# Optimization experiments

Measured on AMD Instinct MI355X. Metric: run time of the kernel, lower is better.

Reference implementation:

```python
import jax, jax.numpy as jnp
import numpy as np

B, T, D = 16, 4096, 768          # batch, tokens, hidden
N_BOX = 1024                      # total boxes across batch
MAX_BBOX = 128                    # cfg.MODEL.MAX_BBOX_NUM
DIM_DETR = 256                    # DETR feature dim (features[:,1:])


def _lin(k, din, dout):
    kw, kb = jax.random.split(k)
    s = 1.0 / np.sqrt(din)
    W = jax.random.uniform(kw, (dout, din), minval=-s, maxval=s, dtype=jnp.float32)
    b = jax.random.uniform(kb, (dout,), minval=-s, maxval=s, dtype=jnp.float32)
    return W, b


def setup_inputs() -> dict:
    key = jax.random.key(0)
    ks = jax.random.split(key, 10)
    inputs = jax.random.normal(ks[0], (B, T, D), dtype=jnp.float32)
    img = jnp.sort(jax.random.randint(ks[1], (N_BOX,), 0, B))
    rest = jax.random.randint(ks[2], (N_BOX, 4), 0, 224)
    bboxes = jnp.concatenate([img[:, None], rest], axis=1).astype(jnp.int32)
    features = jax.random.normal(ks[3], (N_BOX, 1 + DIM_DETR), dtype=jnp.float32)
    t1w, t1b = _lin(ks[4], D, D)      # transform layer 1
    t2w, t2b = _lin(ks[5], D, D)      # transform layer 2
    d1w, d1b = _lin(ks[6], D, D)      # deep_trans layer 1
    d2w, d2b = _lin(ks[7], D, D)      # deep_trans layer 2
    k8a, k8b = jax.random.split(ks[8])
    m1w, m1b = _lin(k8a, DIM_DETR, D) # mlp layer 1 (256->768)
    m2w, m2b = _lin(k8b, D, D)        # mlp layer 2
    pw, pb = _lin(ks[9], 2 * D, D)    # projection (1536->768)
    return dict(inputs=inputs, bboxes=bboxes, features=features,
                t1w=t1w, t1b=t1b, t2w=t2w, t2b=t2b,
                d1w=d1w, d1b=d1b, d2w=d2w, d2b=d2b,
                m1w=m1w, m1b=m1b, m2w=m2w, m2b=m2b,
                pw=pw, pb=pb)


def reference(inputs, bboxes, features, t1w, t1b, t2w, t2b,
              d1w, d1b, d2w, d2b, m1w, m1b, m2w, m2b, pw, pb):
    x = inputs.mean(axis=1)                                    # [B, D]
    ret_x = jax.nn.relu(x @ d1w.T + d1b) @ d2w.T + d2b         # deep_trans
    xt = jax.nn.relu(x @ t1w.T + t1b) @ t2w.T + t2b            # transform
    img = bboxes[:, 0]                                          # [N] image idx per box
    x_boxes = xt[img]                                           # broadcast image feat to its boxes
    fm = jax.nn.relu(features[:, 1:] @ m1w.T + m1b) @ m2w.T + m2b  # DETR mlp
    h = jnp.concatenate([x_boxes, fm], axis=1) @ pw.T + pb      # [N, D]
    # ragged pad: scatter each box into slot (img, rank-within-image)
    counts = jax.ops.segment_sum(jnp.ones((N_BOX,), jnp.int32), img, num_segments=B)
    offsets = jnp.cumsum(counts) - counts                       # exclusive cumsum (boxes sorted by img)
    pos = jnp.arange(N_BOX) - offsets[img]
    vis_output = jnp.zeros((B, MAX_BBOX, D), h.dtype).at[img, pos].set(h)
    att_mask = (jnp.arange(MAX_BBOX)[None, :] < counts[:, None]).astype(jnp.float32)
    return vis_output, att_mask, ret_x
```

## Files before the change

### kernel.cpp

```cpp
#include <hip/hip_runtime.h>

#define B_ 16
#define T_ 4096
#define D_ 768
#define NBOX 1024
#define MAXBB 128
#define DDETR 256

__global__ __launch_bounds__(192) void k_mean_partial(const float4* __restrict__ in4,
                                                      float4* __restrict__ part4) {
    int blk = blockIdx.x;
    int b = blk >> 6;
    int c = blk & 63;
    int t = threadIdx.x;
    const float4* base = in4 + (size_t)b * (T_ * D_ / 4) + (size_t)c * (64 * D_ / 4);
    float4 s = {0.f, 0.f, 0.f, 0.f};
    #pragma unroll 4
    for (int r = 0; r < 64; ++r) {
        float4 v = base[(size_t)r * 192 + t];
        s.x += v.x; s.y += v.y; s.z += v.z; s.w += v.w;
    }
    part4[(size_t)blk * 192 + t] = s;
}

__global__ __launch_bounds__(256) void k_mean_final(const float4* __restrict__ part4,
                                                    float4* __restrict__ x4) {
    int idx = blockIdx.x * 256 + threadIdx.x;
    if (idx >= B_ * 192) return;
    int b = idx / 192;
    int t = idx - b * 192;
    float4 s = {0.f, 0.f, 0.f, 0.f};
    for (int c = 0; c < 64; ++c) {
        float4 v = part4[(size_t)(b * 64 + c) * 192 + t];
        s.x += v.x; s.y += v.y; s.z += v.z; s.w += v.w;
    }
    const float inv = 1.0f / T_;
    s.x *= inv; s.y *= inv; s.z *= inv; s.w *= inv;
    x4[idx] = s;
}

template<int VECA>
__global__ __launch_bounds__(256) void k_gemm64(const float* __restrict__ A, int lda,
                                                const float* __restrict__ W, int ldw,
                                                float* __restrict__ P, int mn,
                                                int N, int K, int lenk) {
    __shared__ float As[16][72];
    __shared__ float Ws[16][72];
    int tid = threadIdx.x;
    int tx = tid & 15, ty = tid >> 4;
    int n0 = blockIdx.x * 64, m0 = blockIdx.y * 64;
    int kb = blockIdx.z * lenk;
    int ke = min(K, kb + lenk);
    int r = tid >> 2, kc = (tid & 3) * 4;

    const float* Ap = A + (size_t)(m0 + r) * lda + kb + kc;
    const float* Wp = W + (size_t)(n0 + r) * ldw + kb + kc;

    float4 acc0 = {0,0,0,0}, acc1 = {0,0,0,0}, acc2 = {0,0,0,0}, acc3 = {0,0,0,0};
    float a0=0,a1=0,a2=0,a3=0, w0=0,w1=0,w2=0,w3=0;

    if (kb < ke) {
        if (VECA) { float4 v = *(const float4*)Ap; a0=v.x; a1=v.y; a2=v.z; a3=v.w; }
        else      { a0=Ap[0]; a1=Ap[1]; a2=Ap[2]; a3=Ap[3]; }
        { float4 v = *(const float4*)Wp; w0=v.x; w1=v.y; w2=v.z; w3=v.w; }

        for (int k0 = kb; k0 < ke; k0 += 16) {
            __syncthreads();
            As[kc+0][r]=a0; As[kc+1][r]=a1; As[kc+2][r]=a2; As[kc+3][r]=a3;
            Ws[kc+0][r]=w0; Ws[kc+1][r]=w1; Ws[kc+2][r]=w2; Ws[kc+3][r]=w3;
            __syncthreads();
            Ap += 16; Wp += 16;
            if (k0 + 16 < ke) {
                if (VECA) { float4 v = *(const float4*)Ap; a0=v.x; a1=v.y; a2=v.z; a3=v.w; }
                else      { a0=Ap[0]; a1=Ap[1]; a2=Ap[2]; a3=Ap[3]; }
                { float4 v = *(const float4*)Wp; w0=v.x; w1=v.y; w2=v.z; w3=v.w; }
            }
            #pragma unroll
            for (int kk = 0; kk < 16; ++kk) {
                float4 av = *(const float4*)&As[kk][ty * 4];
                float4 wv = *(const float4*)&Ws[kk][tx * 4];
                acc0.x += av.x * wv.x; acc0.y += av.x * wv.y; acc0.z += av.x * wv.z; acc0.w += av.x * wv.w;
                acc1.x += av.y * wv.x; acc1.y += av.y * wv.y; acc1.z += av.y * wv.z; acc1.w += av.y * wv.w;
                acc2.x += av.z * wv.x; acc2.y += av.z * wv.y; acc2.z += av.z * wv.z; acc2.w += av.z * wv.w;
                acc3.x += av.w * wv.x; acc3.y += av.w * wv.y; acc3.z += av.w * wv.z; acc3.w += av.w * wv.w;
            }
        }
    }
    float* p = P + (size_t)blockIdx.z * mn + (size_t)(m0 + ty * 4) * N + n0 + tx * 4;
    *(float4*)p = acc0; p += N;
    *(float4*)p = acc1; p += N;
    *(float4*)p = acc2; p += N;
    *(float4*)p = acc3;
}

template<int RELU>
__global__ __launch_bounds__(256) void k_epilogue(const float* __restrict__ P, int mn, int KS,
                                                  const float* __restrict__ bias,
                                                  float* __restrict__ C, int N, int ldc) {
    int idx = blockIdx.x * 256 + threadIdx.x;
    int nf4 = N >> 2;
    int m = idx / nf4;
    int c4 = idx - m * nf4;
    size_t off = (size_t)m * N + c4 * 4;
    float4 s = *(const float4*)&P[off];
    for (int z = 1; z < KS; ++z) {
        float4 t = *(const float4*)&P[(size_t)z * mn + off];
        s.x += t.x; s.y += t.y; s.z += t.z; s.w += t.w;
    }
    float4 b = *(const float4*)&bias[c4 * 4];
    s.x += b.x; s.y += b.y; s.z += b.z; s.w += b.w;
    if (RELU) {
        s.x = fmaxf(s.x, 0.f); s.y = fmaxf(s.y, 0.f);
        s.z = fmaxf(s.z, 0.f); s.w = fmaxf(s.w, 0.f);
    }
    *(float4*)&C[(size_t)m * ldc + c4 * 4] = s;
}

__device__ __forceinline__ void smallM_gemm(const float* __restrict__ A, int lda,
                                            const float* __restrict__ W, int ldw,
                                            const float* __restrict__ bias,
                                            float* __restrict__ C, int ldc,
                                            int K, int relu, int n0) {
    __shared__ float xs[32][17];
    __shared__ float ws_[32][68];
    int tid = threadIdx.x;
    int tx = tid & 63, ty = tid >> 6;
    float acc[4] = {0.f, 0.f, 0.f, 0.f};
    for (int k0 = 0; k0 < K; k0 += 32) {
        __syncthreads();
        #pragma unroll
        for (int i = 0; i < 2; ++i) {
            int e = tid + i * 256;
            int rr = e >> 5, kk = e & 31;
            xs[kk][rr] = A[(size_t)rr * lda + k0 + kk];
        }
        #pragma unroll
        for (int i = 0; i < 2; ++i) {
            int f = tid + i * 256;
            int row = f >> 3, kcc = (f & 7) * 4;
            float4 wv = *(const float4*)(W + (size_t)(n0 + row) * ldw + k0 + kcc);
            ws_[kcc + 0][row] = wv.x; ws_[kcc + 1][row] = wv.y;
            ws_[kcc + 2][row] = wv.z; ws_[kcc + 3][row] = wv.w;
        }
        __syncthreads();
        #pragma unroll
        for (int kk = 0; kk < 32; ++kk) {
            float wv = ws_[kk][tx];
            acc[0] += xs[kk][ty +  0] * wv;
            acc[1] += xs[kk][ty +  4] * wv;
            acc[2] += xs[kk][ty +  8] * wv;
            acc[3] += xs[kk][ty + 12] * wv;
        }
    }
    float bv = bias[n0 + tx];
    #pragma unroll
    for (int i = 0; i < 4; ++i) {
        float v = acc[i] + bv;
        if (relu) v = fmaxf(v, 0.f);
        C[(size_t)(ty + 4 * i) * ldc + n0 + tx] = v;
    }
}

__global__ __launch_bounds__(256) void k_small_l1(const float* __restrict__ x,
                                                  const float* __restrict__ d1w, const float* __restrict__ d1b,
                                                  const float* __restrict__ t1w, const float* __restrict__ t1b,
                                                  float* __restrict__ xcat1) {
    int n0 = blockIdx.x * 64;
    if (blockIdx.y == 0) smallM_gemm(x, D_, d1w, D_, d1b, xcat1,       2 * D_, D_, 1, n0);
    else                 smallM_gemm(x, D_, t1w, D_, t1b, xcat1 + D_,  2 * D_, D_, 1, n0);
}

__global__ __launch_bounds__(256) void k_small_l2(const float* __restrict__ xcat1,
                                                  const float* __restrict__ d2w, const float* __restrict__ d2b,
                                                  const float* __restrict__ t2w, const float* __restrict__ t2b,
                                                  float* __restrict__ retx, float* __restrict__ xt) {
    int n0 = blockIdx.x * 64;
    if (blockIdx.y == 0) smallM_gemm(xcat1,      2 * D_, d2w, D_, d2b, retx, D_, D_, 0, n0);
    else                 smallM_gemm(xcat1 + D_, 2 * D_, t2w, D_, t2b, xt,   D_, D_, 0, n0);
}

__global__ __launch_bounds__(256) void k_gather(const float* __restrict__ xt,
                                                const int* __restrict__ bboxes,
                                                float* __restrict__ hxcat) {
    int idx = blockIdx.x * 256 + threadIdx.x;
    int i = idx / 192, d = idx - i * 192;
    int img = bboxes[i * 5];
    *(float4*)&hxcat[(size_t)i * (2 * D_) + d * 4] =
        *(const float4*)&xt[(size_t)img * D_ + d * 4];
}

__global__ __launch_bounds__(256) void k_meta(const int* __restrict__ bboxes,
                                              int* __restrict__ cnt_g, int* __restrict__ off_g,
                                              float* __restrict__ att) {
    __shared__ int cnt[B_];
    __shared__ int off[B_];
    int tid = threadIdx.x;
    if (tid < B_) cnt[tid] = 0;
    __syncthreads();
    for (int i = tid; i < NBOX; i += 256) atomicAdd(&cnt[bboxes[i * 5]], 1);
    __syncthreads();
    if (tid == 0) {
        int acc = 0;
        for (int b = 0; b < B_; ++b) { off[b] = acc; acc += cnt[b]; }
    }
    __syncthreads();
    if (tid < B_) { cnt_g[tid] = cnt[tid]; off_g[tid] = off[tid]; }
    for (int j = tid; j < B_ * MAXBB; j += 256) {
        int b = j >> 7, p = j & 127;
        att[j] = (p < cnt[b]) ? 1.0f : 0.0f;
    }
}

__global__ __launch_bounds__(256) void k_vis(const float* __restrict__ h,
                                             const int* __restrict__ cnt,
                                             const int* __restrict__ off,
                                             float* __restrict__ vis) {
    int idx = blockIdx.x * 256 + threadIdx.x;
    int slot = idx / 192, d = idx - slot * 192;
    int b = slot >> 7, p = slot & 127;
    float4 v = {0.f, 0.f, 0.f, 0.f};
    if (p < cnt[b]) v = *(const float4*)&h[(size_t)(off[b] + p) * D_ + d * 4];
    *(float4*)&vis[(size_t)slot * D_ + d * 4] = v;
}

extern "C" void kernel_launch(void* const* d_in, const int* in_sizes, int n_in,
                              void* d_out, int out_size, void* d_ws, size_t ws_size,
                              hipStream_t stream) {
    const float* inputs   = (const float*)d_in[0];
    const int*   bboxes   = (const int*)d_in[1];
    const float* features = (const float*)d_in[2];
    const float* t1w = (const float*)d_in[3];
    const float* t1b = (const float*)d_in[4];
    const float* t2w = (const float*)d_in[5];
    const float* t2b = (const float*)d_in[6];
    const float* d1w = (const float*)d_in[7];
    const float* d1b = (const float*)d_in[8];
    const float* d2w = (const float*)d_in[9];
    const float* d2b = (const float*)d_in[10];
    const float* m1w = (const float*)d_in[11];
    const float* m1b = (const float*)d_in[12];
    const float* m2w = (const float*)d_in[13];
    const float* m2b = (const float*)d_in[14];
    const float* pw  = (const float*)d_in[15];
    const float* pb  = (const float*)d_in[16];

    float* out  = (float*)d_out;
    float* vis  = out;
    float* att  = out + 1572864;
    float* retx = out + 1574912;

    const int MN = NBOX * D_;
    float* ws    = (float*)d_ws;
    float* part  = ws;
    float* fm1b  = ws;
    float* x     = part + 786432;
    float* xcat1 = x + 12288;
    float* xt    = xcat1 + 24576;
    float* hxcat = xt + 12288;
    float* h     = hxcat + 1572864;
    int*   cnt   = (int*)(h + 786432);
    int*   off   = cnt + 16;
    float* P     = (float*)(off + 48);

    size_t used_floats = (size_t)(P - ws);
    size_t avail = ws_size / 4 > used_floats ? ws_size / 4 - used_floats : 0;
    int KS = (avail >= (size_t)3 * MN) ? 3 : (avail >= (size_t)2 * MN) ? 2 : 1;

    auto lenk_for = [KS](int K) { return (((K + KS - 1) / KS) + 15) & ~15; };

    k_meta<<<1, 256, 0, stream>>>(bboxes, cnt, off, att);

    k_mean_partial<<<B_ * 64, 192, 0, stream>>>((const float4*)inputs, (float4*)part);
    k_mean_final<<<12, 256, 0, stream>>>((const float4*)part, (float4*)x);

    k_small_l1<<<dim3(12, 2), 256, 0, stream>>>(x, d1w, d1b, t1w, t1b, xcat1);
    k_small_l2<<<dim3(12, 2), 256, 0, stream>>>(xcat1, d2w, d2b, t2w, t2b, retx, xt);

    k_gemm64<0><<<dim3(12, 16, KS), 256, 0, stream>>>(features + 1, 1 + DDETR, m1w, DDETR,
                                                      P, MN, D_, DDETR, lenk_for(DDETR));
    k_epilogue<1><<<768, 256, 0, stream>>>(P, MN, KS, m1b, fm1b, D_, D_);

    k_gemm64<1><<<dim3(12, 16, KS), 256, 0, stream>>>(fm1b, D_, m2w, D_,
                                                      P, MN, D_, D_, lenk_for(D_));
    k_epilogue<0><<<768, 256, 0, stream>>>(P, MN, KS, m2b, hxcat + D_, D_, 2 * D_);

    k_gather<<<768, 256, 0, stream>>>(xt, bboxes, hxcat);

    k_gemm64<1><<<dim3(12, 16, KS), 256, 0, stream>>>(hxcat, 2 * D_, pw, 2 * D_,
                                                      P, MN, D_, 2 * D_, lenk_for(2 * D_));
    k_epilogue<0><<<768, 256, 0, stream>>>(P, MN, KS, pb, h, D_, D_);

    k_vis<<<1536, 256, 0, stream>>>(h, cnt, off, vis);
}
```

Before: 490.8 us.

## Replace FP32 SIMT GEMMs with split-bf16 three-term MFMA GEMMs

Every GEMM now runs on bf16 MFMA instructions. Each fp32 operand is split into hi and lo bf16 parts and three partial products (hh, hl, lh) are summed to approximate fp32 accuracy. Weights, features and intermediate activations are repacked each call into 16-row MFMA tile layouts, and each K-split partial goes to its own slice so epilogues can reduce them and repack. The goal is to move GEMM work off the vector ALUs onto the matrix cores, at the cost of extra pack kernels, more workspace traffic and a small loss of precision.

```diff
diff --git a/kernel.cpp b/kernel.cpp
--- a/kernel.cpp
+++ b/kernel.cpp
@@ -7,11 +7,25 @@
 #define MAXBB 128
 #define DDETR 256
 
+typedef unsigned short u16;
+typedef short bf16x8 __attribute__((ext_vector_type(8)));
+typedef float f32x4 __attribute__((ext_vector_type(4)));
+
+__device__ __forceinline__ void split_bf(float f, u16& h, u16& l) {
+    unsigned u = __builtin_bit_cast(unsigned, f);
+    unsigned r = u + 0x7fffu + ((u >> 16) & 1u);
+    u16 hb = (u16)(r >> 16);
+    float hf = __builtin_bit_cast(float, (unsigned)hb << 16);
+    float lf = f - hf;
+    unsigned ul = __builtin_bit_cast(unsigned, lf);
+    unsigned rl = ul + 0x7fffu + ((ul >> 16) & 1u);
+    h = hb; l = (u16)(rl >> 16);
+}
+
 __global__ __launch_bounds__(192) void k_mean_partial(const float4* __restrict__ in4,
                                                       float4* __restrict__ part4) {
     int blk = blockIdx.x;
-    int b = blk >> 6;
-    int c = blk & 63;
+    int b = blk >> 6, c = blk & 63;
     int t = threadIdx.x;
     const float4* base = in4 + (size_t)b * (T_ * D_ / 4) + (size_t)c * (64 * D_ / 4);
     float4 s = {0.f, 0.f, 0.f, 0.f};
@@ -23,170 +37,295 @@
     part4[(size_t)blk * 192 + t] = s;
 }
 
-__global__ __launch_bounds__(256) void k_mean_final(const float4* __restrict__ part4,
-                                                    float4* __restrict__ x4) {
-    int idx = blockIdx.x * 256 + threadIdx.x;
-    if (idx >= B_ * 192) return;
-    int b = idx / 192;
-    int t = idx - b * 192;
-    float4 s = {0.f, 0.f, 0.f, 0.f};
+__global__ __launch_bounds__(96) void k_mean_final_pack(const float* __restrict__ part,
+                                                        u16* __restrict__ xph, u16* __restrict__ xpl) {
+    int b = blockIdx.x;
+    int kc = threadIdx.x;
+    f32x4 s0 = {0,0,0,0}, s1 = {0,0,0,0};
     for (int c = 0; c < 64; ++c) {
-        float4 v = part4[(size_t)(b * 64 + c) * 192 + t];
-        s.x += v.x; s.y += v.y; s.z += v.z; s.w += v.w;
+        const float* p = part + ((size_t)(b * 64 + c)) * D_ + kc * 8;
+        s0 += *(const f32x4*)p;
+        s1 += *(const f32x4*)(p + 4);
     }
     const float inv = 1.0f / T_;
-    s.x *= inv; s.y *= inv; s.z *= inv; s.w *= inv;
-    x4[idx] = s;
-}
-
-template<int VECA>
-__global__ __launch_bounds__(256) void k_gemm64(const float* __restrict__ A, int lda,
-                                                const float* __restrict__ W, int ldw,
-                                                float* __restrict__ P, int mn,
-                                                int N, int K, int lenk) {
-    __shared__ float As[16][72];
-    __shared__ float Ws[16][72];
-    int tid = threadIdx.x;
-    int tx = tid & 15, ty = tid >> 4;
-    int n0 = blockIdx.x * 64, m0 = blockIdx.y * 64;
-    int kb = blockIdx.z * lenk;
-    int ke = min(K, kb + lenk);
-    int r = tid >> 2, kc = (tid & 3) * 4;
-
-    const float* Ap = A + (size_t)(m0 + r) * lda + kb + kc;
-    const float* Wp = W + (size_t)(n0 + r) * ldw + kb + kc;
-
-    float4 acc0 = {0,0,0,0}, acc1 = {0,0,0,0}, acc2 = {0,0,0,0}, acc3 = {0,0,0,0};
-    float a0=0,a1=0,a2=0,a3=0, w0=0,w1=0,w2=0,w3=0;
-
-    if (kb < ke) {
-        if (VECA) { float4 v = *(const float4*)Ap; a0=v.x; a1=v.y; a2=v.z; a3=v.w; }
-        else      { a0=Ap[0]; a1=Ap[1]; a2=Ap[2]; a3=Ap[3]; }
-        { float4 v = *(const float4*)Wp; w0=v.x; w1=v.y; w2=v.z; w3=v.w; }
-
-        for (int k0 = kb; k0 < ke; k0 += 16) {
-            __syncthreads();
-            As[kc+0][r]=a0; As[kc+1][r]=a1; As[kc+2][r]=a2; As[kc+3][r]=a3;
-            Ws[kc+0][r]=w0; Ws[kc+1][r]=w1; Ws[kc+2][r]=w2; Ws[kc+3][r]=w3;
-            __syncthreads();
-            Ap += 16; Wp += 16;
-            if (k0 + 16 < ke) {
-                if (VECA) { float4 v = *(const float4*)Ap; a0=v.x; a1=v.y; a2=v.z; a3=v.w; }
-                else      { a0=Ap[0]; a1=Ap[1]; a2=Ap[2]; a3=Ap[3]; }
-                { float4 v = *(const float4*)Wp; w0=v.x; w1=v.y; w2=v.z; w3=v.w; }
-            }
+    bf16x8 hv, lv;
+    #pragma unroll
+    for (int j = 0; j < 4; ++j) {
+        u16 h, l;
+        split_bf(s0[j] * inv, h, l); hv[j] = (short)h; lv[j] = (short)l;
+        split_bf(s1[j] * inv, h, l); hv[4 + j] = (short)h; lv[4 + j] = (short)l;
+    }
+    size_t off = ((size_t)kc * 16 + b) * 8;
+    *(bf16x8*)(xph + off) = hv;
+    *(bf16x8*)(xpl + off) = lv;
+}
+
+struct WDesc { const float* src; u16* hi; u16* lo; int N; int K; };
+struct WPack7 { WDesc d[7]; };
+
+__global__ __launch_bounds__(256) void k_pack_w(WPack7 ws) {
+    WDesc d = ws.d[blockIdx.y];
+    int idx = blockIdx.x * 256 + threadIdx.x;
+    int Kc = d.K >> 3;
+    int total = d.N * Kc;
+    if (idx >= total) return;
+    int n = idx / Kc, kc = idx - n * Kc;
+    const float* s = d.src + (size_t)n * d.K + kc * 8;
+    f32x4 v0 = *(const f32x4*)s, v1 = *(const f32x4*)(s + 4);
+    bf16x8 hv, lv;
+    #pragma unroll
+    for (int j = 0; j < 4; ++j) {
+        u16 h, l;
+        split_bf(v0[j], h, l); hv[j] = (short)h; lv[j] = (short)l;
+        split_bf(v1[j], h, l); hv[4 + j] = (short)h; lv[4 + j] = (short)l;
+    }
+    size_t off = ((size_t)(n >> 4) * Kc + kc) * 128 + (n & 15) * 8;
+    *(bf16x8*)(d.hi + off) = hv;
+    *(bf16x8*)(d.lo + off) = lv;
+}
+
+__global__ __launch_bounds__(256) void k_pack_feat(const float* __restrict__ feat,
+                                                   u16* __restrict__ fh, u16* __restrict__ fl) {
+    int idx = blockIdx.x * 256 + threadIdx.x;
+    if (idx >= NBOX * 32) return;
+    int i = idx >> 5, kc = idx & 31;
+    const float* s = feat + (size_t)i * 257 + 1 + kc * 8;
+    bf16x8 hv, lv;
+    #pragma unroll
+    for (int j = 0; j < 8; ++j) {
+        u16 h, l;
+        split_bf(s[j], h, l); hv[j] = (short)h; lv[j] = (short)l;
+    }
+    size_t off = ((size_t)(i >> 4) * 32 + kc) * 128 + (i & 15) * 8;
+    *(bf16x8*)(fh + off) = hv;
+    *(bf16x8*)(fl + off) = lv;
+}
+
+__global__ __launch_bounds__(256) void k_mfma(const u16* __restrict__ Ahi, const u16* __restrict__ Alo,
+                                              const u16* __restrict__ Whi, const u16* __restrict__ Wlo,
+                                              float* __restrict__ P, int Kc, int kcLen, int nks) {
+    int z = blockIdx.z;
+    int term = z / nks, ks = z - term * nks;
+    const u16* A = (term == 2) ? Alo : Ahi;
+    const u16* W = (term == 1) ? Wlo : Whi;
+    int lane = threadIdx.x & 63, w = threadIdx.x >> 6;
+    int wm = w >> 1, wn = w & 1;
+    int mt0 = blockIdx.y * 8 + wm * 4;
+    int nt0 = blockIdx.x * 8 + wn * 4;
+    int kc0 = ks * kcLen;
+    int nk = kcLen >> 2;
+
+    const u16* Ap = A + ((size_t)mt0 * Kc + kc0) * 128 + lane * 8;
+    const u16* Wp = W + ((size_t)nt0 * Kc + kc0) * 128 + lane * 8;
+    size_t astr = (size_t)Kc * 128;
+
+    bf16x8 a[4], b[4];
+    #pragma unroll
+    for (int i = 0; i < 4; ++i) {
+        a[i] = *(const bf16x8*)(Ap + i * astr);
+        b[i] = *(const bf16x8*)(Wp + i * astr);
+    }
+    f32x4 acc[16];
+    #pragma unroll
+    for (int i = 0; i < 16; ++i) acc[i] = (f32x4){0.f, 0.f, 0.f, 0.f};
+
+    for (int k = 0; k < nk; ++k) {
+        bf16x8 an[4], bn[4];
+        if (k + 1 < nk) {
             #pragma unroll
-            for (int kk = 0; kk < 16; ++kk) {
-                float4 av = *(const float4*)&As[kk][ty * 4];
-                float4 wv = *(const float4*)&Ws[kk][tx * 4];
-                acc0.x += av.x * wv.x; acc0.y += av.x * wv.y; acc0.z += av.x * wv.z; acc0.w += av.x * wv.w;
-                acc1.x += av.y * wv.x; acc1.y += av.y * wv.y; acc1.z += av.y * wv.z; acc1.w += av.y * wv.w;
-                acc2.x += av.z * wv.x; acc2.y += av.z * wv.y; acc2.z += av.z * wv.z; acc2.w += av.z * wv.w;
-                acc3.x += av.w * wv.x; acc3.y += av.w * wv.y; acc3.z += av.w * wv.z; acc3.w += av.w * wv.w;
+            for (int i = 0; i < 4; ++i) {
+                an[i] = *(const bf16x8*)(Ap + i * astr + (size_t)(k + 1) * 512);
+                bn[i] = *(const bf16x8*)(Wp + i * astr + (size_t)(k + 1) * 512);
             }
         }
-    }
-    float* p = P + (size_t)blockIdx.z * mn + (size_t)(m0 + ty * 4) * N + n0 + tx * 4;
-    *(float4*)p = acc0; p += N;
-    *(float4*)p = acc1; p += N;
-    *(float4*)p = acc2; p += N;
-    *(float4*)p = acc3;
+        #pragma unroll
+        for (int i = 0; i < 4; ++i)
+            #pragma unroll
+            for (int j = 0; j < 4; ++j)
+                acc[i * 4 + j] = __builtin_amdgcn_mfma_f32_16x16x32_bf16(a[i], b[j], acc[i * 4 + j], 0, 0, 0);
+        #pragma unroll
+        for (int i = 0; i < 4; ++i) { a[i] = an[i]; b[i] = bn[i]; }
+    }
+
+    float* Pz = P + (size_t)z * (1024 * 768);
+    int rb = (lane >> 4) * 4, cb = lane & 15;
+    #pragma unroll
+    for (int i = 0; i < 4; ++i)
+        #pragma unroll
+        for (int j = 0; j < 4; ++j) {
+            int row = (mt0 + i) * 16 + rb;
+            int col = (nt0 + j) * 16 + cb;
+            float* p = Pz + (size_t)row * 768 + col;
+            f32x4 v = acc[i * 4 + j];
+            #pragma unroll
+            for (int r = 0; r < 4; ++r) p[(size_t)r * 768] = v[r];
+        }
 }
 
 template<int RELU>
-__global__ __launch_bounds__(256) void k_epilogue(const float* __restrict__ P, int mn, int KS,
+__global__ __launch_bounds__(256) void k_epi_pack(const float* __restrict__ P, int NS,
                                                   const float* __restrict__ bias,
-                                                  float* __restrict__ C, int N, int ldc) {
-    int idx = blockIdx.x * 256 + threadIdx.x;
-    int nf4 = N >> 2;
-    int m = idx / nf4;
-    int c4 = idx - m * nf4;
-    size_t off = (size_t)m * N + c4 * 4;
-    float4 s = *(const float4*)&P[off];
-    for (int z = 1; z < KS; ++z) {
-        float4 t = *(const float4*)&P[(size_t)z * mn + off];
-        s.x += t.x; s.y += t.y; s.z += t.z; s.w += t.w;
-    }
-    float4 b = *(const float4*)&bias[c4 * 4];
-    s.x += b.x; s.y += b.y; s.z += b.z; s.w += b.w;
-    if (RELU) {
-        s.x = fmaxf(s.x, 0.f); s.y = fmaxf(s.y, 0.f);
-        s.z = fmaxf(s.z, 0.f); s.w = fmaxf(s.w, 0.f);
-    }
-    *(float4*)&C[(size_t)m * ldc + c4 * 4] = s;
-}
-
-__device__ __forceinline__ void smallM_gemm(const float* __restrict__ A, int lda,
-                                            const float* __restrict__ W, int ldw,
-                                            const float* __restrict__ bias,
-                                            float* __restrict__ C, int ldc,
-                                            int K, int relu, int n0) {
-    __shared__ float xs[32][17];
-    __shared__ float ws_[32][68];
-    int tid = threadIdx.x;
-    int tx = tid & 63, ty = tid >> 6;
-    float acc[4] = {0.f, 0.f, 0.f, 0.f};
-    for (int k0 = 0; k0 < K; k0 += 32) {
-        __syncthreads();
-        #pragma unroll
-        for (int i = 0; i < 2; ++i) {
-            int e = tid + i * 256;
-            int rr = e >> 5, kk = e & 31;
-            xs[kk][rr] = A[(size_t)rr * lda + k0 + kk];
+                                                  u16* __restrict__ dhi, u16* __restrict__ dlo,
+                                                  int KcDst, int kcOff) {
+    int idx = blockIdx.x * 256 + threadIdx.x;
+    int m = idx / 96, kc = idx - m * 96;
+    const float* p0 = P + (size_t)m * 768 + kc * 8;
+    f32x4 s0 = *(const f32x4*)p0, s1 = *(const f32x4*)(p0 + 4);
+    for (int z = 1; z < NS; ++z) {
+        const float* p = p0 + (size_t)z * (1024 * 768);
+        s0 += *(const f32x4*)p; s1 += *(const f32x4*)(p + 4);
+    }
+    s0 += *(const f32x4*)(bias + kc * 8);
+    s1 += *(const f32x4*)(bias + kc * 8 + 4);
+    bf16x8 hv, lv;
+    #pragma unroll
+    for (int j = 0; j < 4; ++j) {
+        float v0 = RELU ? fmaxf(s0[j], 0.f) : s0[j];
+        float v1 = RELU ? fmaxf(s1[j], 0.f) : s1[j];
+        u16 h, l;
+        split_bf(v0, h, l); hv[j] = (short)h; lv[j] = (short)l;
+        split_bf(v1, h, l); hv[4 + j] = (short)h; lv[4 + j] = (short)l;
+    }
+    size_t off = ((size_t)(m >> 4) * KcDst + kcOff + kc) * 128 + (m & 15) * 8;
+    *(bf16x8*)(dhi + off) = hv;
+    *(bf16x8*)(dlo + off) = lv;
+}
+
+__global__ __launch_bounds__(256) void k_epi_f32(const float* __restrict__ P, int NS,
+                                                 const float* __restrict__ bias,
+                                                 float* __restrict__ C) {
+    int idx = blockIdx.x * 256 + threadIdx.x;
+    int m = idx / 192, c4 = idx - m * 192;
+    size_t off = (size_t)m * 768 + c4 * 4;
+    f32x4 s = *(const f32x4*)(P + off);
+    for (int z = 1; z < NS; ++z) s += *(const f32x4*)(P + (size_t)z * (1024 * 768) + off);
+    s += *(const f32x4*)(bias + c4 * 4);
+    *(f32x4*)(C + off) = s;
+}
+
+__global__ __launch_bounds__(256) void k_small(const u16* __restrict__ A0h, const u16* __restrict__ A0l,
+                                               const u16* __restrict__ A1h, const u16* __restrict__ A1l,
+                                               const u16* __restrict__ W0h, const u16* __restrict__ W0l,
+                                               const u16* __restrict__ W1h, const u16* __restrict__ W1l,
+                                               float* __restrict__ Ps) {
+    int z = blockIdx.y;
+    int term = z >> 2, ks = z & 3;
+    int lane = threadIdx.x & 63, w = threadIdx.x >> 6;
+    int nt0 = blockIdx.x * 16 + w * 4;
+    int path = nt0 >= 48;
+    int ntp = nt0 - path * 48;
+    const u16* Ah = path ? A1h : A0h;
+    const u16* Al = path ? A1l : A0l;
+    const u16* Wh = path ? W1h : W0h;
+    const u16* Wl = path ? W1l : W0l;
+    const u16* A = (term == 2) ? Al : Ah;
+    const u16* W = (term == 1) ? Wl : Wh;
+    int kc0 = ks * 24;
+
+    const u16* Ap = A + (size_t)kc0 * 128 + lane * 8;
+    const u16* Wp = W + ((size_t)ntp * 96 + kc0) * 128 + lane * 8;
+
+    f32x4 acc[4];
+    #pragma unroll
+    for (int i = 0; i < 4; ++i) acc[i] = (f32x4){0.f, 0.f, 0.f, 0.f};
+
+    #pragma unroll
+    for (int k = 0; k < 6; ++k) {
+        bf16x8 a = *(const bf16x8*)(Ap + (size_t)k * 512);
+        bf16x8 b[4];
+        #pragma unroll
+        for (int j = 0; j < 4; ++j)
+            b[j] = *(const bf16x8*)(Wp + (size_t)j * 96 * 128 + (size_t)k * 512);
+        #pragma unroll
+        for (int j = 0; j < 4; ++j)
+            acc[j] = __builtin_amdgcn_mfma_f32_16x16x32_bf16(a, b[j], acc[j], 0, 0, 0);
+    }
+
+    float* Pz = Ps + (size_t)z * (16 * 1536);
+    int rb = (lane >> 4) * 4, cb = lane & 15;
+    #pragma unroll
+    for (int j = 0; j < 4; ++j) {
+        int col = (nt0 + j) * 16 + cb;
+        float* p = Pz + (size_t)rb * 1536 + col;
+        f32x4 v = acc[j];
+        #pragma unroll
+        for (int r = 0; r < 4; ++r) p[(size_t)r * 1536] = v[r];
+    }
+}
+
+__global__ __launch_bounds__(256) void k_sepi1(const float* __restrict__ Ps,
+                                               const float* __restrict__ d1b, const float* __restrict__ t1b,
+                                               u16* __restrict__ xh, u16* __restrict__ xl) {
+    int idx = blockIdx.x * 256 + threadIdx.x;
+    int r = idx / 192, cc = idx - r * 192;
+    size_t base = (size_t)r * 1536 + cc * 8;
+    f32x4 s0 = {0,0,0,0}, s1 = {0,0,0,0};
+    for (int z = 0; z < 12; ++z) {
+        const float* p = Ps + (size_t)z * (16 * 1536) + base;
+        s0 += *(const f32x4*)p; s1 += *(const f32x4*)(p + 4);
+    }
+    int path = cc >= 96;
+    int ccp = cc - path * 96;
+    const float* bias = (path ? t1b : d1b) + ccp * 8;
+    s0 += *(const f32x4*)bias;
+    s1 += *(const f32x4*)(bias + 4);
+    bf16x8 hv, lv;
+    #pragma unroll
+    for (int j = 0; j < 4; ++j) {
+        u16 h, l;
+        split_bf(fmaxf(s0[j], 0.f), h, l); hv[j] = (short)h; lv[j] = (short)l;
+        split_bf(fmaxf(s1[j], 0.f), h, l); hv[4 + j] = (short)h; lv[4 + j] = (short)l;
+    }
+    size_t off = (size_t)path * 12288 + (size_t)ccp * 128 + r * 8;
+    *(bf16x8*)(xh + off) = hv;
+    *(bf16x8*)(xl + off) = lv;
+}
+
+__global__ __launch_bounds__(256) void k_sepi2(const float* __restrict__ Ps,
+                                               const float* __restrict__ d2b, const float* __restrict__ t2b,
+                                               float* __restrict__ retx,
+                                               u16* __restrict__ xth, u16* __restrict__ xtl) {
+    int idx = blockIdx.x * 256 + threadIdx.x;
+    int r = idx / 192, cc = idx - r * 192;
+    size_t base = (size_t)r * 1536 + cc * 8;
+    f32x4 s0 = {0,0,0,0}, s1 = {0,0,0,0};
+    for (int z = 0; z < 12; ++z) {
+        const float* p = Ps + (size_t)z * (16 * 1536) + base;
+        s0 += *(const f32x4*)p; s1 += *(const f32x4*)(p + 4);
+    }
+    int path = cc >= 96;
+    int ccp = cc - path * 96;
+    const float* bias = (path ? t2b : d2b) + ccp * 8;
+    s0 += *(const f32x4*)bias;
+    s1 += *(const f32x4*)(bias + 4);
+    if (!path) {
+        float* o = retx + (size_t)r * 768 + ccp * 8;
+        *(f32x4*)o = s0;
+        *(f32x4*)(o + 4) = s1;
+    } else {
+        bf16x8 hv, lv;
+        #pragma unroll
+        for (int j = 0; j < 4; ++j) {
+            u16 h, l;
+            split_bf(s0[j], h, l); hv[j] = (short)h; lv[j] = (short)l;
+            split_bf(s1[j], h, l); hv[4 + j] = (short)h; lv[4 + j] = (short)l;
         }
-        #pragma unroll
-        for (int i = 0; i < 2; ++i) {
-            int f = tid + i * 256;
-            int row = f >> 3, kcc = (f & 7) * 4;
-            float4 wv = *(const float4*)(W + (size_t)(n0 + row) * ldw + k0 + kcc);
-            ws_[kcc + 0][row] = wv.x; ws_[kcc + 1][row] = wv.y;
-            ws_[kcc + 2][row] = wv.z; ws_[kcc + 3][row] = wv.w;
-        }
-        __syncthreads();
-        #pragma unroll
-        for (int kk = 0; kk < 32; ++kk) {
-            float wv = ws_[kk][tx];
-            acc[0] += xs[kk][ty +  0] * wv;
-            acc[1] += xs[kk][ty +  4] * wv;
-            acc[2] += xs[kk][ty +  8] * wv;
-            acc[3] += xs[kk][ty + 12] * wv;
-        }
-    }
-    float bv = bias[n0 + tx];
-    #pragma unroll
-    for (int i = 0; i < 4; ++i) {
-        float v = acc[i] + bv;
-        if (relu) v = fmaxf(v, 0.f);
-        C[(size_t)(ty + 4 * i) * ldc + n0 + tx] = v;
-    }
-}
-
-__global__ __launch_bounds__(256) void k_small_l1(const float* __restrict__ x,
-                                                  const float* __restrict__ d1w, const float* __restrict__ d1b,
-                                                  const float* __restrict__ t1w, const float* __restrict__ t1b,
-                                                  float* __restrict__ xcat1) {
-    int n0 = blockIdx.x * 64;
-    if (blockIdx.y == 0) smallM_gemm(x, D_, d1w, D_, d1b, xcat1,       2 * D_, D_, 1, n0);
-    else                 smallM_gemm(x, D_, t1w, D_, t1b, xcat1 + D_,  2 * D_, D_, 1, n0);
-}
-
-__global__ __launch_bounds__(256) void k_small_l2(const float* __restrict__ xcat1,
-                                                  const float* __restrict__ d2w, const float* __restrict__ d2b,
-                                                  const float* __restrict__ t2w, const float* __restrict__ t2b,
-                                                  float* __restrict__ retx, float* __restrict__ xt) {
-    int n0 = blockIdx.x * 64;
-    if (blockIdx.y == 0) smallM_gemm(xcat1,      2 * D_, d2w, D_, d2b, retx, D_, D_, 0, n0);
-    else                 smallM_gemm(xcat1 + D_, 2 * D_, t2w, D_, t2b, xt,   D_, D_, 0, n0);
-}
-
-__global__ __launch_bounds__(256) void k_gather(const float* __restrict__ xt,
-                                                const int* __restrict__ bboxes,
-                                                float* __restrict__ hxcat) {
-    int idx = blockIdx.x * 256 + threadIdx.x;
-    int i = idx / 192, d = idx - i * 192;
+        size_t off = (size_t)ccp * 128 + r * 8;
+        *(bf16x8*)(xth + off) = hv;
+        *(bf16x8*)(xtl + off) = lv;
+    }
+}
+
+__global__ __launch_bounds__(256) void k_gather_pack(const u16* __restrict__ xth, const u16* __restrict__ xtl,
+                                                     const int* __restrict__ bboxes,
+                                                     u16* __restrict__ hxh, u16* __restrict__ hxl) {
+    int idx = blockIdx.x * 256 + threadIdx.x;
+    int i = idx / 96, kc = idx - i * 96;
     int img = bboxes[i * 5];
-    *(float4*)&hxcat[(size_t)i * (2 * D_) + d * 4] =
-        *(const float4*)&xt[(size_t)img * D_ + d * 4];
+    size_t soff = ((size_t)kc * 16 + img) * 8;
+    size_t doff = ((size_t)(i >> 4) * 192 + kc) * 128 + (i & 15) * 8;
+    *(bf16x8*)(hxh + doff) = *(const bf16x8*)(xth + soff);
+    *(bf16x8*)(hxl + doff) = *(const bf16x8*)(xtl + soff);
 }
 
 __global__ __launch_bounds__(256) void k_meta(const int* __restrict__ bboxes,
@@ -249,46 +388,62 @@
     float* att  = out + 1572864;
     float* retx = out + 1574912;
 
-    const int MN = NBOX * D_;
-    float* ws    = (float*)d_ws;
-    float* part  = ws;
-    float* fm1b  = ws;
-    float* x     = part + 786432;
-    float* xcat1 = x + 12288;
-    float* xt    = xcat1 + 24576;
-    float* hxcat = xt + 12288;
-    float* h     = hxcat + 1572864;
-    int*   cnt   = (int*)(h + 786432);
-    int*   off   = cnt + 16;
-    float* P     = (float*)(off + 48);
-
-    size_t used_floats = (size_t)(P - ws);
-    size_t avail = ws_size / 4 > used_floats ? ws_size / 4 - used_floats : 0;
-    int KS = (avail >= (size_t)3 * MN) ? 3 : (avail >= (size_t)2 * MN) ? 2 : 1;
-
-    auto lenk_for = [KS](int K) { return (((K + KS - 1) / KS) + 15) & ~15; };
+    float* wsf  = (float*)d_ws;
+    float* part = wsf;
+    float* P    = wsf + 786432;
+    float* Ps   = P + 12 * 786432;
+    float* h    = Ps + 294912;
+    int*   cnt  = (int*)(h + 786432);
+    int*   off  = cnt + 16;
+    u16*   sb   = (u16*)(off + 48);
+
+    u16* t1wh = sb;              u16* t1wl = t1wh + 589824;
+    u16* t2wh = t1wl + 589824;   u16* t2wl = t2wh + 589824;
+    u16* d1wh = t2wl + 589824;   u16* d1wl = d1wh + 589824;
+    u16* d2wh = d1wl + 589824;   u16* d2wl = d2wh + 589824;
+    u16* m1wh = d2wl + 589824;   u16* m1wl = m1wh + 196608;
+    u16* m2wh = m1wl + 196608;   u16* m2wl = m2wh + 589824;
+    u16* pwh  = m2wl + 589824;   u16* pwl  = pwh + 1179648;
+    u16* feah = pwl + 1179648;   u16* feal = feah + 262144;
+    u16* fm1h = feal + 262144;   u16* fm1l = fm1h + 786432;
+    u16* hxh  = fm1l + 786432;   u16* hxl  = hxh + 1572864;
+    u16* xph  = hxl + 1572864;   u16* xpl  = xph + 12288;
+    u16* xch  = xpl + 12288;     u16* xcl  = xch + 24576;
+    u16* xth  = xcl + 24576;     u16* xtl  = xth + 12288;
 
     k_meta<<<1, 256, 0, stream>>>(bboxes, cnt, off, att);
 
     k_mean_partial<<<B_ * 64, 192, 0, stream>>>((const float4*)inputs, (float4*)part);
-    k_mean_final<<<12, 256, 0, stream>>>((const float4*)part, (float4*)x);
-
-    k_small_l1<<<dim3(12, 2), 256, 0, stream>>>(x, d1w, d1b, t1w, t1b, xcat1);
-    k_small_l2<<<dim3(12, 2), 256, 0, stream>>>(xcat1, d2w, d2b, t2w, t2b, retx, xt);
-
-    k_gemm64<0><<<dim3(12, 16, KS), 256, 0, stream>>>(features + 1, 1 + DDETR, m1w, DDETR,
-                                                      P, MN, D_, DDETR, lenk_for(DDETR));
-    k_epilogue<1><<<768, 256, 0, stream>>>(P, MN, KS, m1b, fm1b, D_, D_);
-
-    k_gemm64<1><<<dim3(12, 16, KS), 256, 0, stream>>>(fm1b, D_, m2w, D_,
-                                                      P, MN, D_, D_, lenk_for(D_));
-    k_epilogue<0><<<768, 256, 0, stream>>>(P, MN, KS, m2b, hxcat + D_, D_, 2 * D_);
-
-    k_gather<<<768, 256, 0, stream>>>(xt, bboxes, hxcat);
-
-    k_gemm64<1><<<dim3(12, 16, KS), 256, 0, stream>>>(hxcat, 2 * D_, pw, 2 * D_,
-                                                      P, MN, D_, 2 * D_, lenk_for(2 * D_));
-    k_epilogue<0><<<768, 256, 0, stream>>>(P, MN, KS, pb, h, D_, D_);
+    k_mean_final_pack<<<16, 96, 0, stream>>>(part, xph, xpl);
+
+    WPack7 wp;
+    wp.d[0] = {t1w, t1wh, t1wl, 768, 768};
+    wp.d[1] = {t2w, t2wh, t2wl, 768, 768};
+    wp.d[2] = {d1w, d1wh, d1wl, 768, 768};
+    wp.d[3] = {d2w, d2wh, d2wl, 768, 768};
+    wp.d[4] = {m1w, m1wh, m1wl, 768, 256};
+    wp.d[5] = {m2w, m2wh, m2wl, 768, 768};
+    wp.d[6] = {pw,  pwh,  pwl,  768, 1536};
+    k_pack_w<<<dim3(576, 7), 256, 0, stream>>>(wp);
+    k_pack_feat<<<128, 256, 0, stream>>>(features, feah, feal);
+
+    k_small<<<dim3(6, 12), 256, 0, stream>>>(xph, xpl, xph, xpl,
+                                             d1wh, d1wl, t1wh, t1wl, Ps);
+    k_sepi1<<<12, 256, 0, stream>>>(Ps, d1b, t1b, xch, xcl);
+    k_small<<<dim3(6, 12), 256, 0, stream>>>(xch, xcl, xch + 12288, xcl + 12288,
+                                             d2wh, d2wl, t2wh, t2wl, Ps);
+    k_sepi2<<<12, 256, 0, stream>>>(Ps, d2b, t2b, retx, xth, xtl);
+
+    k_gather_pack<<<384, 256, 0, stream>>>(xth, xtl, bboxes, hxh, hxl);
+
+    k_mfma<<<dim3(6, 8, 6), 256, 0, stream>>>(feah, feal, m1wh, m1wl, P, 32, 16, 2);
+    k_epi_pack<1><<<384, 256, 0, stream>>>(P, 6, m1b, fm1h, fm1l, 96, 0);
+
+    k_mfma<<<dim3(6, 8, 12), 256, 0, stream>>>(fm1h, fm1l, m2wh, m2wl, P, 96, 24, 4);
+    k_epi_pack<0><<<384, 256, 0, stream>>>(P, 12, m2b, hxh, hxl, 192, 96);
+
+    k_mfma<<<dim3(6, 8, 12), 256, 0, stream>>>(hxh, hxl, pwh, pwl, P, 192, 48, 4);
+    k_epi_f32<<<768, 256, 0, stream>>>(P, 12, pb, h);
 
     k_vis<<<1536, 256, 0, stream>>>(h, cnt, off, vis);
 }
```

After: 427.2 us. -12.9%, faster.
